# Optimization experiments

Hardware: AMD Instinct MI355X
Metric: run time of the kernel (lower is better)

The kernel has to match this reference:

```python
import jax, jax.numpy as jnp
import numpy as np

N, F_IN, E = 50000, 128, 800000
HID, HEADS, EMB = 32, 8, 64
NEG_SLOPE = 0.2


def gat_conv(x, src, dst, W_src, W_dst, att_src, att_dst, bias, heads, out_ch, concat):
    n = x.shape[0]
    h_src = (x @ W_src).reshape(n, heads, out_ch)   # [N,H,C]
    h_dst = (x @ W_dst).reshape(n, heads, out_ch)
    a_src = jnp.sum(h_src * att_src, axis=-1)       # [N,H]
    a_dst = jnp.sum(h_dst * att_dst, axis=-1)
    e = jax.nn.leaky_relu(a_src[src] + a_dst[dst], NEG_SLOPE)  # [E,H]
    # segment softmax over destination nodes (stable, max detached as in PyG)
    m = jax.ops.segment_max(e, dst, num_segments=n)
    m = jnp.where(jnp.isfinite(m), m, 0.0)
    ex = jnp.exp(e - jax.lax.stop_gradient(m)[dst])
    denom = jax.ops.segment_sum(ex, dst, num_segments=n)
    alpha = ex / (denom[dst] + 1e-16)               # [E,H]
    msg = h_src[src] * alpha[:, :, None]            # [E,H,C]
    out = jax.ops.segment_sum(msg, dst, num_segments=n)  # [N,H,C]
    if concat:
        out = out.reshape(n, heads * out_ch)
    else:
        out = out.mean(axis=1)
    return out + bias


def setup_inputs() -> dict:
    key = jax.random.key(0)
    ks = jax.random.split(key, 12)
    g = lambda k, shape: jax.random.normal(k, shape, dtype=jnp.float32) * (1.0 / np.sqrt(shape[0]))
    x = jax.random.normal(ks[0], (N, F_IN), dtype=jnp.float32)
    edge_index = jax.random.randint(ks[1], (2, E), 0, N, dtype=jnp.int64)
    return {
        "x": x,
        "edge_index": edge_index,
        "W_src1": g(ks[2], (F_IN, HEADS * HID)),
        "W_dst1": g(ks[3], (F_IN, HEADS * HID)),
        "att_src1": g(ks[4], (HEADS, HID)) * 0.1,
        "att_dst1": g(ks[5], (HEADS, HID)) * 0.1,
        "b1": jnp.zeros((HEADS * HID,), dtype=jnp.float32),
        "W_src2": g(ks[6], (HEADS * HID, EMB)),
        "W_dst2": g(ks[7], (HEADS * HID, EMB)),
        "att_src2": g(ks[8], (1, EMB)) * 0.1,
        "att_dst2": g(ks[9], (1, EMB)) * 0.1,
        "b2": jnp.zeros((EMB,), dtype=jnp.float32),
    }


def reference(x, edge_index, W_src1, W_dst1, att_src1, att_dst1, b1,
              W_src2, W_dst2, att_src2, att_dst2, b2):
    src, dst = edge_index[0], edge_index[1]
    h = gat_conv(x, src, dst, W_src1, W_dst1, att_src1, att_dst1, b1, HEADS, HID, True)
    h = jax.nn.relu(h)
    out = gat_conv(h, src, dst, W_src2, W_dst2, att_src2, att_dst2, b2, 1, EMB, False)
    return out
```

## Files before the change

kernel.cpp:

```cpp
#include <hip/hip_runtime.h>
#include <hip/hip_bf16.h>
#include <cstdint>
#include <cstddef>

#define NN    50000
#define FIN   128
#define EE    800000
#define HID_  32
#define HEADS_ 8
#define EMB_  64
#define NEG   0.2f
#define NB_SCAN 196

typedef short bf16x8 __attribute__((ext_vector_type(8)));
typedef float f32x4  __attribute__((ext_vector_type(4)));

static __device__ __forceinline__ float lrelu(float v){ return v < 0.f ? NEG * v : v; }
static __device__ __forceinline__ ushort f2bf(float f){
    uint u = __float_as_uint(f);
    uint r = (u + 0x7FFFu + ((u >> 16) & 1u)) >> 16;
    return (ushort)r;
}
static __device__ __forceinline__ float bf2f(ushort u){
    return __uint_as_float(((uint)u) << 16);
}

__global__ void k_build_wt1(const float* __restrict__ Wsrc, const float* __restrict__ Wdst,
                            const float* __restrict__ asrc, const float* __restrict__ adst,
                            ushort* __restrict__ wt1bf){
    int idx = blockIdx.x * blockDim.x + threadIdx.x;
    if (idx >= FIN * 16) return;
    int f = idx >> 4, j = idx & 15;
    const float* W; const float* a; int h;
    if (j < 8) { W = Wsrc; a = asrc; h = j; } else { W = Wdst; a = adst; h = j - 8; }
    float s = 0.f;
    #pragma unroll
    for (int c = 0; c < HID_; ++c)
        s += W[(size_t)f * (HEADS_ * HID_) + h * HID_ + c] * a[h * HID_ + c];
    wt1bf[j * 128 + f] = f2bf(s);
}

__global__ void k_build_wt2(const float* __restrict__ Wsrc, const float* __restrict__ Wdst,
                            const float* __restrict__ asrc, const float* __restrict__ adst,
                            float* __restrict__ wt2){
    int idx = blockIdx.x * blockDim.x + threadIdx.x;
    if (idx >= 256 * 2) return;
    int f = idx >> 1, j = idx & 1;
    const float* W = j ? Wdst : Wsrc;
    const float* a = j ? adst : asrc;
    float s = 0.f;
    #pragma unroll
    for (int c = 0; c < EMB_; ++c) s += W[(size_t)f * EMB_ + c] * a[c];
    wt2[j * 256 + f] = s;
}

__global__ void k_prep_w1t(const float* __restrict__ W, ushort* __restrict__ w1t){
    int idx = blockIdx.x * blockDim.x + threadIdx.x;
    if (idx >= 256 * 128) return;
    int n = idx >> 7, k = idx & 127;
    w1t[idx] = f2bf(W[(size_t)k * 256 + n]);
}

__global__ void k_prep_w2t(const float* __restrict__ W, ushort* __restrict__ w2t){
    int idx = blockIdx.x * blockDim.x + threadIdx.x;
    if (idx >= 64 * 256) return;
    int n = idx >> 8, k = idx & 255;
    w2t[idx] = f2bf(W[(size_t)k * 64 + n]);
}

__global__ void k_hist(const int* __restrict__ dst, int* __restrict__ deg, int* __restrict__ rank){
    int e = blockIdx.x * blockDim.x + threadIdx.x;
    if (e < EE) rank[e] = atomicAdd(&deg[dst[e]], 1);
}

__global__ __launch_bounds__(256) void k_scan1(const int* __restrict__ deg,
                                               int* __restrict__ pre, int* __restrict__ bsum){
    __shared__ int s[256];
    int tid = threadIdx.x;
    int i = blockIdx.x * 256 + tid;
    int v = (i < NN) ? deg[i] : 0;
    s[tid] = v;
    __syncthreads();
    #pragma unroll
    for (int off = 1; off < 256; off <<= 1){
        int t = (tid >= off) ? s[tid - off] : 0;
        __syncthreads();
        s[tid] += t;
        __syncthreads();
    }
    if (i < NN) pre[i] = s[tid] - v;
    if (tid == 255) bsum[blockIdx.x] = s[255];
}

__global__ __launch_bounds__(256) void k_scan2(const int* __restrict__ bsum,
                                               int* __restrict__ boff, int* __restrict__ row_ptr){
    __shared__ int s[256];
    int tid = threadIdx.x;
    int v = (tid < NB_SCAN) ? bsum[tid] : 0;
    s[tid] = v;
    __syncthreads();
    #pragma unroll
    for (int off = 1; off < 256; off <<= 1){
        int t = (tid >= off) ? s[tid - off] : 0;
        __syncthreads();
        s[tid] += t;
        __syncthreads();
    }
    if (tid < NB_SCAN) boff[tid] = s[tid] - v;
    if (tid == 255) row_ptr[NN] = s[255];
}

__global__ __launch_bounds__(256) void k_scan3(const int* __restrict__ pre, const int* __restrict__ boff,
                                               int* __restrict__ row_ptr){
    int i = blockIdx.x * 256 + threadIdx.x;
    if (i < NN) row_ptr[i] = pre[i] + boff[blockIdx.x];
}

__global__ void k_scatter(const int* __restrict__ src, const int* __restrict__ dst,
                          const int* __restrict__ row_ptr, const int* __restrict__ rank,
                          int* __restrict__ col){
    int e = blockIdx.x * blockDim.x + threadIdx.x;
    if (e < EE){
        int d = dst[e];
        col[row_ptr[d] + rank[e]] = src[e];
    }
}

__global__ __launch_bounds__(256) void k_gemm1_mfma(const float* __restrict__ x,
                                                    const ushort* __restrict__ w1t,
                                                    const ushort* __restrict__ wt1bf,
                                                    ushort* __restrict__ c,
                                                    float* __restrict__ a_src1,
                                                    float* __restrict__ a_dst1){
    __shared__ ushort As[64][136];
    __shared__ ushort Bs[128][136];
    __shared__ ushort Bsa[16][136];
    const int tid = threadIdx.x;
    const int m0 = blockIdx.x * 64;
    const int n0 = blockIdx.y * 128;
    #pragma unroll
    for (int i = 0; i < 8; ++i){
        int idx = tid + i * 256;
        int r = idx >> 5, c4 = idx & 31;
        int m = m0 + r;
        float4 v = make_float4(0.f, 0.f, 0.f, 0.f);
        if (m < NN) v = *(const float4*)&x[(size_t)m * FIN + c4 * 4];
        ushort4 u; u.x = f2bf(v.x); u.y = f2bf(v.y); u.z = f2bf(v.z); u.w = f2bf(v.w);
        *(ushort4*)&As[r][c4 * 4] = u;
    }
    #pragma unroll
    for (int i = 0; i < 8; ++i){
        int idx = tid + i * 256;
        int r = idx >> 4, c8 = idx & 15;
        const ushort4* s4 = (const ushort4*)&w1t[(size_t)(n0 + r) * 128 + c8 * 8];
        *(ushort4*)&Bs[r][c8 * 8]     = s4[0];
        *(ushort4*)&Bs[r][c8 * 8 + 4] = s4[1];
    }
    if (blockIdx.y == 0){
        int r = tid >> 4, c8 = tid & 15;
        const ushort4* s4 = (const ushort4*)&wt1bf[r * 128 + c8 * 8];
        *(ushort4*)&Bsa[r][c8 * 8]     = s4[0];
        *(ushort4*)&Bsa[r][c8 * 8 + 4] = s4[1];
    }
    __syncthreads();
    const int lane = tid & 63;
    const int w    = tid >> 6;
    const int mr   = lane & 15;
    const int kg   = lane >> 4;
    f32x4 acc[8];
    #pragma unroll
    for (int i = 0; i < 8; ++i) acc[i] = (f32x4){0.f, 0.f, 0.f, 0.f};
    f32x4 acca = (f32x4){0.f, 0.f, 0.f, 0.f};
    #pragma unroll
    for (int ks = 0; ks < 4; ++ks){
        bf16x8 a = *(const bf16x8*)&As[w * 16 + mr][ks * 32 + kg * 8];
        #pragma unroll
        for (int nf = 0; nf < 8; ++nf){
            bf16x8 b = *(const bf16x8*)&Bs[nf * 16 + mr][ks * 32 + kg * 8];
            acc[nf] = __builtin_amdgcn_mfma_f32_16x16x32_bf16(a, b, acc[nf], 0, 0, 0);
        }
        if (blockIdx.y == 0){
            bf16x8 ba = *(const bf16x8*)&Bsa[mr][ks * 32 + kg * 8];
            acca = __builtin_amdgcn_mfma_f32_16x16x32_bf16(a, ba, acca, 0, 0, 0);
        }
    }
    #pragma unroll
    for (int nf = 0; nf < 8; ++nf){
        int colb = n0 + nf * 16 + mr;
        #pragma unroll
        for (int r = 0; r < 4; ++r){
            int row = m0 + w * 16 + kg * 4 + r;
            if (row < NN) c[(size_t)row * 256 + colb] = f2bf(acc[nf][r]);
        }
    }
    if (blockIdx.y == 0){
        int j = mr;
        #pragma unroll
        for (int r = 0; r < 4; ++r){
            int row = m0 + w * 16 + kg * 4 + r;
            if (row < NN){
                if (j < 8) a_src1[(size_t)row * 8 + j]       = acca[r];
                else       a_dst1[(size_t)row * 8 + (j - 8)] = acca[r];
            }
        }
    }
}

__global__ __launch_bounds__(256) void k_gemm2_mfma(const ushort* __restrict__ hbf,
                                                    const ushort* __restrict__ w2t,
                                                    ushort* __restrict__ c2){
    __shared__ ushort As[64][264];
    __shared__ ushort Bs[64][264];
    const int tid = threadIdx.x;
    const int m0 = blockIdx.x * 64;
    #pragma unroll
    for (int i = 0; i < 8; ++i){
        int idx = tid + i * 256;
        int r = idx >> 5, c8 = idx & 31;
        int m = m0 + r;
        ushort4 v0 = make_ushort4(0,0,0,0), v1 = make_ushort4(0,0,0,0);
        if (m < NN){
            const ushort4* s4 = (const ushort4*)&hbf[(size_t)m * 256 + c8 * 8];
            v0 = s4[0]; v1 = s4[1];
        }
        *(ushort4*)&As[r][c8 * 8]     = v0;
        *(ushort4*)&As[r][c8 * 8 + 4] = v1;
    }
    #pragma unroll
    for (int i = 0; i < 8; ++i){
        int idx = tid + i * 256;
        int r = idx >> 5, c8 = idx & 31;
        const ushort4* s4 = (const ushort4*)&w2t[(size_t)r * 256 + c8 * 8];
        *(ushort4*)&Bs[r][c8 * 8]     = s4[0];
        *(ushort4*)&Bs[r][c8 * 8 + 4] = s4[1];
    }
    __syncthreads();
    const int lane = tid & 63;
    const int w    = tid >> 6;
    const int mr   = lane & 15;
    const int kg   = lane >> 4;
    f32x4 acc[4];
    #pragma unroll
    for (int i = 0; i < 4; ++i) acc[i] = (f32x4){0.f, 0.f, 0.f, 0.f};
    #pragma unroll
    for (int ks = 0; ks < 8; ++ks){
        bf16x8 a = *(const bf16x8*)&As[w * 16 + mr][ks * 32 + kg * 8];
        #pragma unroll
        for (int nf = 0; nf < 4; ++nf){
            bf16x8 b = *(const bf16x8*)&Bs[nf * 16 + mr][ks * 32 + kg * 8];
            acc[nf] = __builtin_amdgcn_mfma_f32_16x16x32_bf16(a, b, acc[nf], 0, 0, 0);
        }
    }
    #pragma unroll
    for (int nf = 0; nf < 4; ++nf){
        int colb = nf * 16 + mr;
        #pragma unroll
        for (int r = 0; r < 4; ++r){
            int row = m0 + w * 16 + kg * 4 + r;
            if (row < NN) c2[(size_t)row * 64 + colb] = f2bf(acc[nf][r]);
        }
    }
}

__global__ __launch_bounds__(256) void k_agg1(const ushort* __restrict__ hsrc, const float* __restrict__ a_src,
                                              const float* __restrict__ a_dst, const int* __restrict__ row_ptr,
                                              const int* __restrict__ col, const float* __restrict__ b1,
                                              const float* __restrict__ wt2,
                                              ushort* __restrict__ hout_bf,
                                              float* __restrict__ a_src2, float* __restrict__ a_dst2){
    int node = blockIdx.x * 4 + (threadIdx.x >> 6);
    if (node >= NN) return;
    int lane = threadIdx.x & 63;
    int head = lane >> 3;
    float ad = a_dst[(size_t)node * 8 + head];
    const ushort4* h4 = (const ushort4*)hsrc;
    float4 acc = make_float4(0.f, 0.f, 0.f, 0.f);
    float den = 0.f;
    int b = row_ptr[node], en = row_ptr[node + 1];
    int i = b;
    for (; i + 4 <= en; i += 4){
        int s0 = col[i], s1 = col[i+1], s2 = col[i+2], s3 = col[i+3];
        float e0 = a_src[(size_t)s0 * 8 + head];
        float e1 = a_src[(size_t)s1 * 8 + head];
        float e2 = a_src[(size_t)s2 * 8 + head];
        float e3 = a_src[(size_t)s3 * 8 + head];
        ushort4 v0 = h4[(size_t)s0 * 64 + lane];
        ushort4 v1 = h4[(size_t)s1 * 64 + lane];
        ushort4 v2 = h4[(size_t)s2 * 64 + lane];
        ushort4 v3 = h4[(size_t)s3 * 64 + lane];
        float p0 = __expf(lrelu(e0 + ad));
        float p1 = __expf(lrelu(e1 + ad));
        float p2 = __expf(lrelu(e2 + ad));
        float p3 = __expf(lrelu(e3 + ad));
        acc.x += p0*bf2f(v0.x) + p1*bf2f(v1.x) + p2*bf2f(v2.x) + p3*bf2f(v3.x);
        acc.y += p0*bf2f(v0.y) + p1*bf2f(v1.y) + p2*bf2f(v2.y) + p3*bf2f(v3.y);
        acc.z += p0*bf2f(v0.z) + p1*bf2f(v1.z) + p2*bf2f(v2.z) + p3*bf2f(v3.z);
        acc.w += p0*bf2f(v0.w) + p1*bf2f(v1.w) + p2*bf2f(v2.w) + p3*bf2f(v3.w);
        den += p0 + p1 + p2 + p3;
    }
    for (; i < en; ++i){
        int s = col[i];
        float p = __expf(lrelu(a_src[(size_t)s * 8 + head] + ad));
        ushort4 v = h4[(size_t)s * 64 + lane];
        acc.x += p * bf2f(v.x); acc.y += p * bf2f(v.y);
        acc.z += p * bf2f(v.z); acc.w += p * bf2f(v.w);
        den += p;
    }
    float inv = 1.f / (den + 1e-16f);
    float4 bb = ((const float4*)b1)[lane];
    float4 o;
    o.x = fmaxf(acc.x * inv + bb.x, 0.f);
    o.y = fmaxf(acc.y * inv + bb.y, 0.f);
    o.z = fmaxf(acc.z * inv + bb.z, 0.f);
    o.w = fmaxf(acc.w * inv + bb.w, 0.f);
    ushort4 ob; ob.x = f2bf(o.x); ob.y = f2bf(o.y); ob.z = f2bf(o.z); ob.w = f2bf(o.w);
    ((ushort4*)hout_bf)[(size_t)node * 64 + lane] = ob;
    float4 ws4 = ((const float4*)wt2)[lane];
    float4 wd4 = ((const float4*)(wt2 + 256))[lane];
    float ss = o.x*ws4.x + o.y*ws4.y + o.z*ws4.z + o.w*ws4.w;
    float sd = o.x*wd4.x + o.y*wd4.y + o.z*wd4.z + o.w*wd4.w;
    #pragma unroll
    for (int off = 32; off > 0; off >>= 1){
        ss += __shfl_xor(ss, off);
        sd += __shfl_xor(sd, off);
    }
    if (lane == 0){ a_src2[node] = ss; a_dst2[node] = sd; }
}

__global__ __launch_bounds__(256) void k_agg2(const ushort* __restrict__ h2bf, const float* __restrict__ a_src2,
                                              const float* __restrict__ a_dst2, const int* __restrict__ row_ptr,
                                              const int* __restrict__ col, const float* __restrict__ b2,
                                              float* __restrict__ out){
    int node = blockIdx.x * 4 + (threadIdx.x >> 6);
    if (node >= NN) return;
    int lane = threadIdx.x & 63;
    float ad = a_dst2[node];
    float acc = 0.f, den = 0.f;
    int b = row_ptr[node], en = row_ptr[node + 1];
    int i = b;
    for (; i + 4 <= en; i += 4){
        int s0 = col[i], s1 = col[i+1], s2 = col[i+2], s3 = col[i+3];
        float e0 = a_src2[s0], e1 = a_src2[s1], e2 = a_src2[s2], e3 = a_src2[s3];
        ushort u0 = h2bf[(size_t)s0 * 64 + lane];
        ushort u1 = h2bf[(size_t)s1 * 64 + lane];
        ushort u2 = h2bf[(size_t)s2 * 64 + lane];
        ushort u3 = h2bf[(size_t)s3 * 64 + lane];
        float p0 = __expf(lrelu(e0 + ad));
        float p1 = __expf(lrelu(e1 + ad));
        float p2 = __expf(lrelu(e2 + ad));
        float p3 = __expf(lrelu(e3 + ad));
        acc += p0*bf2f(u0) + p1*bf2f(u1) + p2*bf2f(u2) + p3*bf2f(u3);
        den += p0 + p1 + p2 + p3;
    }
    for (; i < en; ++i){
        int s = col[i];
        float p = __expf(lrelu(a_src2[s] + ad));
        acc += p * bf2f(h2bf[(size_t)s * 64 + lane]);
        den += p;
    }
    out[(size_t)node * 64 + lane] = acc / (den + 1e-16f) + b2[lane];
}

extern "C" void kernel_launch(void* const* d_in, const int* in_sizes, int n_in,
                              void* d_out, int out_size, void* d_ws, size_t ws_size,
                              hipStream_t stream){
    const float* x        = (const float*)d_in[0];
    const int*   ei       = (const int*)  d_in[1];
    const float* Wsrc1    = (const float*)d_in[2];
    const float* Wdst1    = (const float*)d_in[3];
    const float* att_src1 = (const float*)d_in[4];
    const float* att_dst1 = (const float*)d_in[5];
    const float* b1       = (const float*)d_in[6];
    const float* Wsrc2    = (const float*)d_in[7];
    const float* Wdst2    = (const float*)d_in[8];
    const float* att_src2 = (const float*)d_in[9];
    const float* att_dst2 = (const float*)d_in[10];
    const float* b2       = (const float*)d_in[11];
    float* out = (float*)d_out;
    const int* srcp = ei;
    const int* dstp = ei + EE;

    char* base = (char*)d_ws;
    ushort* hbf1   = (ushort*)base;  base += (size_t)NN * 256 * 2;
    ushort* hrel   = (ushort*)base;  base += (size_t)NN * 256 * 2;
    ushort* h2bf   = (ushort*)base;  base += (size_t)NN * 64 * 2;
    float*  a_src1 = (float*)base;   base += (size_t)NN * 8 * 4;
    float*  a_dst1 = (float*)base;   base += (size_t)NN * 8 * 4;
    float*  a_src2 = (float*)base;   base += (size_t)NN * 4;
    float*  a_dst2 = (float*)base;   base += (size_t)NN * 4;
    ushort* wt1bf  = (ushort*)base;  base += 2048 * 2;
    float*  wt2    = (float*)base;   base += 512 * 4;
    ushort* w1t    = (ushort*)base;  base += 32768 * 2;
    ushort* w2t    = (ushort*)base;  base += 16384 * 2;
    int* deg     = (int*)base;       base += (size_t)NN * 4;
    int* row_ptr = (int*)base;       base += (size_t)(NN + 1) * 4;
    int* rank    = (int*)base;       base += (size_t)EE * 4;
    int* col     = (int*)base;       base += (size_t)EE * 4;
    int* pre     = (int*)base;       base += (size_t)NN * 4;
    int* bsum    = (int*)base;       base += 256 * 4;
    int* boff    = (int*)base;       base += 256 * 4;

    hipMemsetAsync(deg, 0, NN * sizeof(int), stream);

    k_build_wt1<<<8, 256, 0, stream>>>(Wsrc1, Wdst1, att_src1, att_dst1, wt1bf);
    k_build_wt2<<<2, 256, 0, stream>>>(Wsrc2, Wdst2, att_src2, att_dst2, wt2);
    k_prep_w1t<<<128, 256, 0, stream>>>(Wsrc1, w1t);
    k_prep_w2t<<<64, 256, 0, stream>>>(Wsrc2, w2t);

    k_hist<<<(EE + 255) / 256, 256, 0, stream>>>(dstp, deg, rank);
    k_scan1<<<NB_SCAN, 256, 0, stream>>>(deg, pre, bsum);
    k_scan2<<<1, 256, 0, stream>>>(bsum, boff, row_ptr);
    k_scan3<<<NB_SCAN, 256, 0, stream>>>(pre, boff, row_ptr);
    k_scatter<<<(EE + 255) / 256, 256, 0, stream>>>(srcp, dstp, row_ptr, rank, col);

    dim3 g1((NN + 63) / 64, 2);
    k_gemm1_mfma<<<g1, 256, 0, stream>>>(x, w1t, wt1bf, hbf1, a_src1, a_dst1);

    k_agg1<<<(NN + 3) / 4, 256, 0, stream>>>(hbf1, a_src1, a_dst1, row_ptr, col, b1, wt2,
                                             hrel, a_src2, a_dst2);

    k_gemm2_mfma<<<(NN + 63) / 64, 256, 0, stream>>>(hrel, w2t, h2bf);

    k_agg2<<<(NN + 3) / 4, 256, 0, stream>>>(h2bf, a_src2, a_dst2, row_ptr, col, b2, out);
}
```

Before: 215.3 us.

## Merge prep kernels, single-pass scan, exp2 softmax, deeper gather unroll

Folds the four weight-prep kernels into one launch and replaces the three-kernel scan with one kernel that uses decoupled lookback flags. The attention weights are pre-scaled by log2(e) so the aggregations can use the hardware exp2 and a max-based leaky ReLU. The edge loops in both aggregation kernels are unrolled to 8 edges so more gathers are in flight. This cuts launch count and ALU work, at the cost of a spin-wait that assumes all earlier scan blocks are resident, plus more register pressure.

```diff
diff --git a/kernel.cpp b/kernel.cpp
--- a/kernel.cpp
+++ b/kernel.cpp
@@ -11,11 +11,11 @@
 #define EMB_  64
 #define NEG   0.2f
 #define NB_SCAN 196
+#define LOG2E 1.4426950408889634f
 
 typedef short bf16x8 __attribute__((ext_vector_type(8)));
 typedef float f32x4  __attribute__((ext_vector_type(4)));
 
-static __device__ __forceinline__ float lrelu(float v){ return v < 0.f ? NEG * v : v; }
 static __device__ __forceinline__ ushort f2bf(float f){
     uint u = __float_as_uint(f);
     uint r = (u + 0x7FFFu + ((u >> 16) & 1u)) >> 16;
@@ -24,48 +24,44 @@
 static __device__ __forceinline__ float bf2f(ushort u){
     return __uint_as_float(((uint)u) << 16);
 }
-
-__global__ void k_build_wt1(const float* __restrict__ Wsrc, const float* __restrict__ Wdst,
-                            const float* __restrict__ asrc, const float* __restrict__ adst,
-                            ushort* __restrict__ wt1bf){
+static __device__ __forceinline__ float pexp(float t){
+    return __builtin_amdgcn_exp2f(fmaxf(t, NEG * t));
+}
+
+__global__ __launch_bounds__(256) void k_prep(const float* __restrict__ Wsrc1, const float* __restrict__ Wdst1,
+                                              const float* __restrict__ asrc1, const float* __restrict__ adst1,
+                                              const float* __restrict__ Wsrc2, const float* __restrict__ Wdst2,
+                                              const float* __restrict__ asrc2, const float* __restrict__ adst2,
+                                              ushort* __restrict__ wt1bf, float* __restrict__ wt2,
+                                              ushort* __restrict__ w1t, ushort* __restrict__ w2t){
     int idx = blockIdx.x * blockDim.x + threadIdx.x;
-    if (idx >= FIN * 16) return;
-    int f = idx >> 4, j = idx & 15;
-    const float* W; const float* a; int h;
-    if (j < 8) { W = Wsrc; a = asrc; h = j; } else { W = Wdst; a = adst; h = j - 8; }
-    float s = 0.f;
-    #pragma unroll
-    for (int c = 0; c < HID_; ++c)
-        s += W[(size_t)f * (HEADS_ * HID_) + h * HID_ + c] * a[h * HID_ + c];
-    wt1bf[j * 128 + f] = f2bf(s);
-}
-
-__global__ void k_build_wt2(const float* __restrict__ Wsrc, const float* __restrict__ Wdst,
-                            const float* __restrict__ asrc, const float* __restrict__ adst,
-                            float* __restrict__ wt2){
-    int idx = blockIdx.x * blockDim.x + threadIdx.x;
-    if (idx >= 256 * 2) return;
-    int f = idx >> 1, j = idx & 1;
-    const float* W = j ? Wdst : Wsrc;
-    const float* a = j ? adst : asrc;
-    float s = 0.f;
-    #pragma unroll
-    for (int c = 0; c < EMB_; ++c) s += W[(size_t)f * EMB_ + c] * a[c];
-    wt2[j * 256 + f] = s;
-}
-
-__global__ void k_prep_w1t(const float* __restrict__ W, ushort* __restrict__ w1t){
-    int idx = blockIdx.x * blockDim.x + threadIdx.x;
-    if (idx >= 256 * 128) return;
-    int n = idx >> 7, k = idx & 127;
-    w1t[idx] = f2bf(W[(size_t)k * 256 + n]);
-}
-
-__global__ void k_prep_w2t(const float* __restrict__ W, ushort* __restrict__ w2t){
-    int idx = blockIdx.x * blockDim.x + threadIdx.x;
-    if (idx >= 64 * 256) return;
-    int n = idx >> 8, k = idx & 255;
-    w2t[idx] = f2bf(W[(size_t)k * 64 + n]);
+    if (idx < 2048){
+        int f = idx >> 4, j = idx & 15;
+        const float* W; const float* a; int h;
+        if (j < 8) { W = Wsrc1; a = asrc1; h = j; } else { W = Wdst1; a = adst1; h = j - 8; }
+        float s = 0.f;
+        #pragma unroll
+        for (int c = 0; c < HID_; ++c)
+            s += W[(size_t)f * (HEADS_ * HID_) + h * HID_ + c] * a[h * HID_ + c];
+        wt1bf[j * 128 + f] = f2bf(s * LOG2E);
+    } else if (idx < 2560){
+        int t = idx - 2048;
+        int f = t >> 1, j = t & 1;
+        const float* W = j ? Wdst2 : Wsrc2;
+        const float* a = j ? adst2 : asrc2;
+        float s = 0.f;
+        #pragma unroll
+        for (int c = 0; c < EMB_; ++c) s += W[(size_t)f * EMB_ + c] * a[c];
+        wt2[j * 256 + f] = s * LOG2E;
+    } else if (idx < 35328){
+        int t = idx - 2560;
+        int n = t >> 7, k = t & 127;
+        w1t[t] = f2bf(Wsrc1[(size_t)k * 256 + n]);
+    } else if (idx < 51712){
+        int t = idx - 35328;
+        int n = t >> 8, k = t & 255;
+        w2t[t] = f2bf(Wsrc2[(size_t)k * 64 + n]);
+    }
 }
 
 __global__ void k_hist(const int* __restrict__ dst, int* __restrict__ deg, int* __restrict__ rank){
@@ -73,11 +69,12 @@
     if (e < EE) rank[e] = atomicAdd(&deg[dst[e]], 1);
 }
 
-__global__ __launch_bounds__(256) void k_scan1(const int* __restrict__ deg,
-                                               int* __restrict__ pre, int* __restrict__ bsum){
+__global__ __launch_bounds__(256) void k_scanall(const int* __restrict__ deg, int* __restrict__ row_ptr,
+                                                 int* __restrict__ bsum, int* __restrict__ flags){
     __shared__ int s[256];
-    int tid = threadIdx.x;
-    int i = blockIdx.x * 256 + tid;
+    __shared__ int ps[256];
+    int tid = threadIdx.x, b = blockIdx.x;
+    int i = b * 256 + tid;
     int v = (i < NN) ? deg[i] : 0;
     s[tid] = v;
     __syncthreads();
@@ -88,32 +85,25 @@
         s[tid] += t;
         __syncthreads();
     }
-    if (i < NN) pre[i] = s[tid] - v;
-    if (tid == 255) bsum[blockIdx.x] = s[255];
-}
-
-__global__ __launch_bounds__(256) void k_scan2(const int* __restrict__ bsum,
-                                               int* __restrict__ boff, int* __restrict__ row_ptr){
-    __shared__ int s[256];
-    int tid = threadIdx.x;
-    int v = (tid < NB_SCAN) ? bsum[tid] : 0;
-    s[tid] = v;
+    if (tid == 255){
+        bsum[b] = s[255];
+        __hip_atomic_store(&flags[b], 1, __ATOMIC_RELEASE, __HIP_MEMORY_SCOPE_AGENT);
+    }
+    int p = 0;
+    if (tid < b){
+        while (__hip_atomic_load(&flags[tid], __ATOMIC_ACQUIRE, __HIP_MEMORY_SCOPE_AGENT) == 0){}
+        p = bsum[tid];
+    }
+    ps[tid] = p;
     __syncthreads();
     #pragma unroll
-    for (int off = 1; off < 256; off <<= 1){
-        int t = (tid >= off) ? s[tid - off] : 0;
+    for (int off = 128; off > 0; off >>= 1){
+        if (tid < off) ps[tid] += ps[tid + off];
         __syncthreads();
-        s[tid] += t;
-        __syncthreads();
-    }
-    if (tid < NB_SCAN) boff[tid] = s[tid] - v;
-    if (tid == 255) row_ptr[NN] = s[255];
-}
-
-__global__ __launch_bounds__(256) void k_scan3(const int* __restrict__ pre, const int* __restrict__ boff,
-                                               int* __restrict__ row_ptr){
-    int i = blockIdx.x * 256 + threadIdx.x;
-    if (i < NN) row_ptr[i] = pre[i] + boff[blockIdx.x];
+    }
+    int boff = ps[0];
+    if (i < NN) row_ptr[i] = boff + s[tid] - v;
+    if (b == 0 && tid == 0) row_ptr[NN] = EE;
 }
 
 __global__ void k_scatter(const int* __restrict__ src, const int* __restrict__ dst,
@@ -278,29 +268,28 @@
     float den = 0.f;
     int b = row_ptr[node], en = row_ptr[node + 1];
     int i = b;
-    for (; i + 4 <= en; i += 4){
-        int s0 = col[i], s1 = col[i+1], s2 = col[i+2], s3 = col[i+3];
-        float e0 = a_src[(size_t)s0 * 8 + head];
-        float e1 = a_src[(size_t)s1 * 8 + head];
-        float e2 = a_src[(size_t)s2 * 8 + head];
-        float e3 = a_src[(size_t)s3 * 8 + head];
-        ushort4 v0 = h4[(size_t)s0 * 64 + lane];
-        ushort4 v1 = h4[(size_t)s1 * 64 + lane];
-        ushort4 v2 = h4[(size_t)s2 * 64 + lane];
-        ushort4 v3 = h4[(size_t)s3 * 64 + lane];
-        float p0 = __expf(lrelu(e0 + ad));
-        float p1 = __expf(lrelu(e1 + ad));
-        float p2 = __expf(lrelu(e2 + ad));
-        float p3 = __expf(lrelu(e3 + ad));
-        acc.x += p0*bf2f(v0.x) + p1*bf2f(v1.x) + p2*bf2f(v2.x) + p3*bf2f(v3.x);
-        acc.y += p0*bf2f(v0.y) + p1*bf2f(v1.y) + p2*bf2f(v2.y) + p3*bf2f(v3.y);
-        acc.z += p0*bf2f(v0.z) + p1*bf2f(v1.z) + p2*bf2f(v2.z) + p3*bf2f(v3.z);
-        acc.w += p0*bf2f(v0.w) + p1*bf2f(v1.w) + p2*bf2f(v2.w) + p3*bf2f(v3.w);
-        den += p0 + p1 + p2 + p3;
+    for (; i + 8 <= en; i += 8){
+        int ss[8]; float e[8]; ushort4 v[8]; float p[8];
+        #pragma unroll
+        for (int j = 0; j < 8; ++j) ss[j] = col[i + j];
+        #pragma unroll
+        for (int j = 0; j < 8; ++j) e[j] = a_src[(size_t)ss[j] * 8 + head];
+        #pragma unroll
+        for (int j = 0; j < 8; ++j) v[j] = h4[(size_t)ss[j] * 64 + lane];
+        #pragma unroll
+        for (int j = 0; j < 8; ++j) p[j] = pexp(e[j] + ad);
+        #pragma unroll
+        for (int j = 0; j < 8; ++j){
+            acc.x += p[j] * bf2f(v[j].x);
+            acc.y += p[j] * bf2f(v[j].y);
+            acc.z += p[j] * bf2f(v[j].z);
+            acc.w += p[j] * bf2f(v[j].w);
+            den += p[j];
+        }
     }
     for (; i < en; ++i){
         int s = col[i];
-        float p = __expf(lrelu(a_src[(size_t)s * 8 + head] + ad));
+        float p = pexp(a_src[(size_t)s * 8 + head] + ad);
         ushort4 v = h4[(size_t)s * 64 + lane];
         acc.x += p * bf2f(v.x); acc.y += p * bf2f(v.y);
         acc.z += p * bf2f(v.z); acc.w += p * bf2f(v.w);
@@ -317,14 +306,14 @@
     ((ushort4*)hout_bf)[(size_t)node * 64 + lane] = ob;
     float4 ws4 = ((const float4*)wt2)[lane];
     float4 wd4 = ((const float4*)(wt2 + 256))[lane];
-    float ss = o.x*ws4.x + o.y*ws4.y + o.z*ws4.z + o.w*ws4.w;
-    float sd = o.x*wd4.x + o.y*wd4.y + o.z*wd4.z + o.w*wd4.w;
+    float ss2 = o.x*ws4.x + o.y*ws4.y + o.z*ws4.z + o.w*ws4.w;
+    float sd2 = o.x*wd4.x + o.y*wd4.y + o.z*wd4.z + o.w*wd4.w;
     #pragma unroll
     for (int off = 32; off > 0; off >>= 1){
-        ss += __shfl_xor(ss, off);
-        sd += __shfl_xor(sd, off);
-    }
-    if (lane == 0){ a_src2[node] = ss; a_dst2[node] = sd; }
+        ss2 += __shfl_xor(ss2, off);
+        sd2 += __shfl_xor(sd2, off);
+    }
+    if (lane == 0){ a_src2[node] = ss2; a_dst2[node] = sd2; }
 }
 
 __global__ __launch_bounds__(256) void k_agg2(const ushort* __restrict__ h2bf, const float* __restrict__ a_src2,
@@ -338,23 +327,25 @@
     float acc = 0.f, den = 0.f;
     int b = row_ptr[node], en = row_ptr[node + 1];
     int i = b;
-    for (; i + 4 <= en; i += 4){
-        int s0 = col[i], s1 = col[i+1], s2 = col[i+2], s3 = col[i+3];
-        float e0 = a_src2[s0], e1 = a_src2[s1], e2 = a_src2[s2], e3 = a_src2[s3];
-        ushort u0 = h2bf[(size_t)s0 * 64 + lane];
-        ushort u1 = h2bf[(size_t)s1 * 64 + lane];
-        ushort u2 = h2bf[(size_t)s2 * 64 + lane];
-        ushort u3 = h2bf[(size_t)s3 * 64 + lane];
-        float p0 = __expf(lrelu(e0 + ad));
-        float p1 = __expf(lrelu(e1 + ad));
-        float p2 = __expf(lrelu(e2 + ad));
-        float p3 = __expf(lrelu(e3 + ad));
-        acc += p0*bf2f(u0) + p1*bf2f(u1) + p2*bf2f(u2) + p3*bf2f(u3);
-        den += p0 + p1 + p2 + p3;
+    for (; i + 8 <= en; i += 8){
+        int ss[8]; float e[8]; ushort u[8]; float p[8];
+        #pragma unroll
+        for (int j = 0; j < 8; ++j) ss[j] = col[i + j];
+        #pragma unroll
+        for (int j = 0; j < 8; ++j) e[j] = a_src2[ss[j]];
+        #pragma unroll
+        for (int j = 0; j < 8; ++j) u[j] = h2bf[(size_t)ss[j] * 64 + lane];
+        #pragma unroll
+        for (int j = 0; j < 8; ++j) p[j] = pexp(e[j] + ad);
+        #pragma unroll
+        for (int j = 0; j < 8; ++j){
+            acc += p[j] * bf2f(u[j]);
+            den += p[j];
+        }
     }
     for (; i < en; ++i){
         int s = col[i];
-        float p = __expf(lrelu(a_src2[s] + ad));
+        float p = pexp(a_src2[s] + ad);
         acc += p * bf2f(h2bf[(size_t)s * 64 + lane]);
         den += p;
     }
@@ -393,24 +384,20 @@
     ushort* w1t    = (ushort*)base;  base += 32768 * 2;
     ushort* w2t    = (ushort*)base;  base += 16384 * 2;
     int* deg     = (int*)base;       base += (size_t)NN * 4;
+    int* flags   = (int*)base;       base += 256 * 4;
     int* row_ptr = (int*)base;       base += (size_t)(NN + 1) * 4;
     int* rank    = (int*)base;       base += (size_t)EE * 4;
     int* col     = (int*)base;       base += (size_t)EE * 4;
-    int* pre     = (int*)base;       base += (size_t)NN * 4;
     int* bsum    = (int*)base;       base += 256 * 4;
-    int* boff    = (int*)base;       base += 256 * 4;
-
-    hipMemsetAsync(deg, 0, NN * sizeof(int), stream);
-
-    k_build_wt1<<<8, 256, 0, stream>>>(Wsrc1, Wdst1, att_src1, att_dst1, wt1bf);
-    k_build_wt2<<<2, 256, 0, stream>>>(Wsrc2, Wdst2, att_src2, att_dst2, wt2);
-    k_prep_w1t<<<128, 256, 0, stream>>>(Wsrc1, w1t);
-    k_prep_w2t<<<64, 256, 0, stream>>>(Wsrc2, w2t);
+
+    hipMemsetAsync(deg, 0, (NN + 256) * sizeof(int), stream);
+
+    k_prep<<<202, 256, 0, stream>>>(Wsrc1, Wdst1, att_src1, att_dst1,
+                                    Wsrc2, Wdst2, att_src2, att_dst2,
+                                    wt1bf, wt2, w1t, w2t);
 
     k_hist<<<(EE + 255) / 256, 256, 0, stream>>>(dstp, deg, rank);
-    k_scan1<<<NB_SCAN, 256, 0, stream>>>(deg, pre, bsum);
-    k_scan2<<<1, 256, 0, stream>>>(bsum, boff, row_ptr);
-    k_scan3<<<NB_SCAN, 256, 0, stream>>>(pre, boff, row_ptr);
+    k_scanall<<<NB_SCAN, 256, 0, stream>>>(deg, row_ptr, bsum, flags);
     k_scatter<<<(EE + 255) / 256, 256, 0, stream>>>(srcp, dstp, row_ptr, rank, col);
 
     dim3 g1((NN + 63) / 64, 2);
```

After: 217.2 us. About the same (+0.9%).
